# Performance work log

Hardware: AMD Instinct MI355X
Metric: run time of the kernel (lower is better)

The kernel has to match this reference:

```python
import jax, jax.numpy as jnp
import numpy as np

K = 8            # top-k neighbors per channel
BN_EPS = 1e-3    # keras BatchNormalization default


def top_k_features(h, adj, k):
    # h: [N, F], adj: [N, N] (dense). Per node and per channel, take the k
    # largest masked neighbor feature values, then prepend the node's own feature.
    masked = adj[:, None, :] * h.T[None, :, :]        # [N, F, N]
    topk = jax.lax.top_k(masked, k)[0]                # [N, F, K]
    topk = jnp.transpose(topk, (0, 2, 1))             # [N, K, F]
    return jnp.concatenate([h[:, None, :], topk], axis=1)  # [N, K+1, F]


def conv1d(x, w):
    # x: [N, L, Cin], w: [kw, Cin, Cout], VALID 1D conv
    return jax.lax.conv_general_dilated(x, w, (1,), 'VALID',
                                        dimension_numbers=('NWC', 'WIO', 'NWC'))


def batchnorm(x, gamma, beta, mean, var):
    return gamma * (x - mean) * jax.lax.rsqrt(var + BN_EPS) + beta


def setup_inputs():
    key = jax.random.key(0)
    ks = jax.random.split(key, 16)
    N, Fin, H, Cout, NF = 1600, 1433, 32, 7, 8
    x = jax.random.normal(ks[0], (N, Fin), jnp.float32)
    # sparse binary adjacency, avg degree ~16
    adj = (jax.random.uniform(ks[1], (N, N)) < 0.01).astype(jnp.float32)
    mask = jax.random.uniform(ks[2], (N,)) < 0.5

    def g(k, shape, fan_in):
        return jax.random.normal(k, shape, jnp.float32) * (1.0 / np.sqrt(fan_in))

    W0 = g(ks[3], (Fin, H), Fin)                 # DenseConvolution (GCN) weight
    # LGConv block 1: F=32 -> mid (32+8)//2=20 -> 8; kernels 5,5 reduce 9->5->1
    W1a = g(ks[4], (5, 32, 20), 5 * 32)
    W1b = g(ks[5], (5, 20, NF), 5 * 20)
    # LGConv block 2: F=40 -> mid (40+8)//2=24 -> 8
    W2a = g(ks[6], (5, 40, 24), 5 * 40)
    W2b = g(ks[7], (5, 24, NF), 5 * 24)
    Wout = g(ks[8], (H + 2 * NF, Cout), H + 2 * NF)  # 48 -> 7
    bn = {}
    for i, kk in ((1, 9), (2, 12)):
        bn[f'g{i}'] = 1.0 + 0.1 * jax.random.normal(ks[kk], (NF,), jnp.float32)
        bn[f'b{i}'] = 0.1 * jax.random.normal(ks[kk + 1], (NF,), jnp.float32)
        bn[f'm{i}'] = 0.1 * jax.random.normal(ks[kk + 2], (NF,), jnp.float32)
        bn[f'v{i}'] = jax.random.uniform(ks[kk], (NF,), jnp.float32, 0.5, 1.5)
    return {'x': x, 'adj': adj, 'W0': W0, 'W1a': W1a, 'W1b': W1b,
            'W2a': W2a, 'W2b': W2b, 'Wout': Wout,
            'g1': bn['g1'], 'b1': bn['b1'], 'm1': bn['m1'], 'v1': bn['v1'],
            'g2': bn['g2'], 'b2': bn['b2'], 'm2': bn['m2'], 'v2': bn['v2'],
            'mask': mask}


def reference(x, adj, W0, W1a, W1b, W2a, W2b, Wout,
              g1, b1, m1, v1, g2, b2, m2, v2, mask):
    # inference mode: dropout = identity
    h = adj @ (x @ W0)                                # GCN layer, hidden=32
    for Wa, Wb, g, b, m, v in ((W1a, W1b, g1, b1, m1, v1),
                               (W2a, W2b, g2, b2, m2, v2)):
        t = top_k_features(h, adj, K)                 # [N, K+1, F]
        c = conv1d(t, Wa)                             # [N, 5, mid]
        c = conv1d(c, Wb)[:, 0, :]                    # [N, 8]
        c = batchnorm(c, g, b, m, v)
        h = jnp.concatenate([h, c], axis=-1)          # 32 -> 40 -> 48
    logits = adj @ (h @ Wout)                         # [N, 7]
    # Mask layer (boolean_mask); static-shape variant: zero out masked rows
    return jnp.where(mask[:, None], logits, 0.0)
```

## Files before the change

kernel.cpp:

```cpp
#include <hip/hip_runtime.h>


constexpr int NN   = 1600;
constexpr int FIN  = 1433;
constexpr int HGCN = 32;
constexpr int NBS  = 96;
constexpr float BN_EPS = 1e-3f;

constexpr int KS    = 16;
constexpr int CHUNK = 90;
constexpr int BM    = 32;
constexpr int SXS   = 92;
constexpr int RB    = NN / BM;
constexpr int CSRB  = 400;
constexpr int K1B   = CSRB + 1 + RB * KS;
constexpr int GB    = 256;
constexpr int NT    = 512;

__device__ __forceinline__ void astore(float* p, float v) {
    __hip_atomic_store(p, v, __ATOMIC_RELAXED, __HIP_MEMORY_SCOPE_AGENT);
}

__device__ __forceinline__ void gbar(int* cnt, int* rel, int phase) {
    __syncthreads();
    if (blockIdx.x == 0) {
        if (threadIdx.x == 0)
            __hip_atomic_fetch_add(&cnt[phase * 1024], 1,
                                   __ATOMIC_RELAXED, __HIP_MEMORY_SCOPE_AGENT);
        if (threadIdx.x < 32) {
            int* slot = &cnt[phase * 1024 + threadIdx.x * 32];
            while (__hip_atomic_load(slot, __ATOMIC_RELAXED,
                                     __HIP_MEMORY_SCOPE_AGENT) < (GB / 32))
                __builtin_amdgcn_s_sleep(1);
        }
        if (threadIdx.x == 0)
            __hip_atomic_store(&rel[phase], 1,
                               __ATOMIC_RELAXED, __HIP_MEMORY_SCOPE_AGENT);
    } else {
        if (threadIdx.x == 0) {
            __hip_atomic_fetch_add(&cnt[phase * 1024 + (blockIdx.x & 31) * 32], 1,
                                   __ATOMIC_RELAXED, __HIP_MEMORY_SCOPE_AGENT);
            while (__hip_atomic_load(&rel[phase], __ATOMIC_RELAXED,
                                     __HIP_MEMORY_SCOPE_AGENT) == 0)
                __builtin_amdgcn_s_sleep(1);
        }
    }
    __syncthreads();
}

__global__ __launch_bounds__(256) void k1(const float* __restrict__ x,
                                          const float* __restrict__ W0,
                                          const float* __restrict__ adj,
                                          const float* __restrict__ W1a,
                                          const float* __restrict__ W2a,
                                          int* __restrict__ deg,
                                          unsigned short* __restrict__ nbr,
                                          const unsigned char* __restrict__ mb,
                                          int* __restrict__ flag,
                                          float* __restrict__ wsT1,
                                          float* __restrict__ wsT2,
                                          float* __restrict__ h0) {
    __shared__ float sx[BM][SXS];
    __shared__ float sw[CHUNK * HGCN];
    int b = blockIdx.x, t = threadIdx.x;

    if (b < CSRB) {
        int lane = t & 63;
        int row  = b * 4 + (t >> 6);
        const float*  ar  = adj + (size_t)row * NN;
        const float4* ar4 = (const float4*)ar;
        unsigned short* nb = nbr + (size_t)row * NBS;
        int cnt = 0;
        #pragma unroll
        for (int it = 0; it < 6; ++it) {
            float4 v = ar4[it * 64 + lane];
            int base = it * 256 + 4 * lane;
            #pragma unroll
            for (int c = 0; c < 4; ++c) {
                float vc = (c == 0) ? v.x : (c == 1) ? v.y : (c == 2) ? v.z : v.w;
                bool p = (vc != 0.0f);
                unsigned long long m = __ballot(p);
                if (p) {
                    int off = cnt + __popcll(m & ((1ull << lane) - 1ull));
                    if (off < NBS) nb[off] = (unsigned short)(base + c);
                }
                cnt += __popcll(m);
            }
        }
        {
            float v = ar[1536 + lane];
            bool p = (v != 0.0f);
            unsigned long long m = __ballot(p);
            if (p) {
                int off = cnt + __popcll(m & ((1ull << lane) - 1ull));
                if (off < NBS) nb[off] = (unsigned short)(1536 + lane);
            }
            cnt += __popcll(m);
        }
        if (lane == 0) deg[row] = cnt < NBS ? cnt : NBS;
        return;
    }

    if (b == CSRB) {
        if (t < 64) {
            int lane = t;
            bool odd = false, flt = false;
            for (int i = lane; i < NN; i += 64) {
                unsigned char v = mb[i];
                if (v) {
                    int r = i & 3;
                    if (r != 0) odd = true;
                    if (r >= 2 && (v == 0x3F || v == 0x80)) flt = true;
                }
            }
            unsigned long long mo = __ballot(odd);
            unsigned long long mf = __ballot(flt);
            if (lane == 0) *flag = mf ? 2 : (mo ? 1 : 0);
        }
        for (int s = t; s < 5 * 32 * 20; s += 256) {
            int kw = s / 640, r = s - kw * 640, ci = r / 20, o = r - ci * 20;
            wsT1[(kw * 20 + o) * 36 + ci] = W1a[s];
        }
        for (int s = t; s < 5 * 40 * 24; s += 256) {
            int kw = s / 960, r = s - kw * 960, ci = r / 24, o = r - ci * 24;
            wsT2[(kw * 24 + o) * 44 + ci] = W2a[s];
        }
        return;
    }

    int tile = b - (CSRB + 1);
    int rb   = tile % RB;
    int ks   = tile / RB;
    int lane = t & 31;
    int row0 = rb * BM;
    int k0   = ks * CHUNK;
    int vk   = FIN - k0; if (vk > CHUNK) vk = CHUNK;

    {
        int g = t >> 5;
        #pragma unroll
        for (int j = 0; j < 4; ++j) {
            int r = g + 8 * j;
            const float* xr = x + (size_t)(row0 + r) * FIN + k0;
            #pragma unroll
            for (int m = 0; m < 3; ++m) {
                int k = lane + 32 * m;
                if (k < CHUNK) sx[r][k] = (k < vk) ? xr[k] : 0.0f;
            }
        }
    }
    {
        const float4* w4  = (const float4*)(W0 + (size_t)k0 * HGCN);
        float4*       sw4 = (float4*)sw;
        int vf4 = vk * 8;
        for (int i = t; i < CHUNK * 8; i += 256)
            sw4[i] = (i < vf4) ? w4[i] : make_float4(0.f, 0.f, 0.f, 0.f);
    }
    __syncthreads();

    int col = lane;
    int rq  = t >> 5;
    float acc0 = 0.f, acc1 = 0.f, acc2 = 0.f, acc3 = 0.f;
    #pragma unroll 4
    for (int kk = 0; kk < 88; kk += 4) {
        float4 a0 = *(const float4*)&sx[rq     ][kk];
        float4 a1 = *(const float4*)&sx[rq +  8][kk];
        float4 a2 = *(const float4*)&sx[rq + 16][kk];
        float4 a3 = *(const float4*)&sx[rq + 24][kk];
        float w0v = sw[(kk + 0) * HGCN + col];
        float w1v = sw[(kk + 1) * HGCN + col];
        float w2v = sw[(kk + 2) * HGCN + col];
        float w3v = sw[(kk + 3) * HGCN + col];
        acc0 += a0.x * w0v + a0.y * w1v + a0.z * w2v + a0.w * w3v;
        acc1 += a1.x * w0v + a1.y * w1v + a1.z * w2v + a1.w * w3v;
        acc2 += a2.x * w0v + a2.y * w1v + a2.z * w2v + a2.w * w3v;
        acc3 += a3.x * w0v + a3.y * w1v + a3.z * w2v + a3.w * w3v;
    }
    #pragma unroll
    for (int kk = 88; kk < CHUNK; ++kk) {
        float wv = sw[kk * HGCN + col];
        acc0 += sx[rq     ][kk] * wv;
        acc1 += sx[rq +  8][kk] * wv;
        acc2 += sx[rq + 16][kk] * wv;
        acc3 += sx[rq + 24][kk] * wv;
    }

    atomicAdd(&h0[(row0 + rq     ) * HGCN + col], acc0);
    atomicAdd(&h0[(row0 + rq +  8) * HGCN + col], acc1);
    atomicAdd(&h0[(row0 + rq + 16) * HGCN + col], acc2);
    atomicAdd(&h0[(row0 + rq + 24) * HGCN + col], acc3);
}

template<int F, int MID, int FP>
__device__ __forceinline__ void lgconv_phase(int b, int wave, int lane,
        const int* __restrict__ deg, const unsigned short* __restrict__ nbr,
        const float* sWt, const float* __restrict__ Wb,
        const float* __restrict__ g, const float* __restrict__ bb,
        const float* __restrict__ mm, const float* __restrict__ vv,
        const float* __restrict__ h32, const float* __restrict__ c1in,
        float* __restrict__ outbuf, float* T, float* C1) {
    int row = b + 256 * wave;
    if (row >= NN) return;
    int d = deg[row];
    const unsigned short* nb = nbr + (size_t)row * NBS;

    if (lane < F) {
        float t0=0.f,t1=0.f,t2=0.f,t3=0.f,t4=0.f,t5=0.f,t6=0.f,t7=0.f;
        #define BUBBLE(val_) { float val=val_, c;                       \
            c = t0; t0 = fmaxf(c, val); val = fminf(c, val);            \
            c = t1; t1 = fmaxf(c, val); val = fminf(c, val);            \
            c = t2; t2 = fmaxf(c, val); val = fminf(c, val);            \
            c = t3; t3 = fmaxf(c, val); val = fminf(c, val);            \
            c = t4; t4 = fmaxf(c, val); val = fminf(c, val);            \
            c = t5; t5 = fmaxf(c, val); val = fminf(c, val);            \
            c = t6; t6 = fmaxf(c, val); val = fminf(c, val);            \
            c = t7; t7 = fmaxf(c, val); val = fminf(c, val); }
        #define LDV(n_) ((F == 32) ? h32[(n_) * HGCN + lane]            \
            : ((lane < 32) ? h32[(n_) * HGCN + lane] : c1in[(n_) * 8 + (lane - 32)]))
        int it = 0;
        for (; it + 8 <= d; it += 8) {
            float v[8];
            #pragma unroll
            for (int j = 0; j < 8; ++j) v[j] = LDV((int)nb[it + j]);
            #pragma unroll
            for (int j = 0; j < 8; ++j) BUBBLE(v[j]);
        }
        for (; it < d; ++it) BUBBLE(LDV((int)nb[it]));
        T[0*F+lane] = LDV(row);
        T[1*F+lane] = t0; T[2*F+lane] = t1; T[3*F+lane] = t2; T[4*F+lane] = t3;
        T[5*F+lane] = t4; T[6*F+lane] = t5; T[7*F+lane] = t6; T[8*F+lane] = t7;
        #undef LDV
        #undef BUBBLE
    }
    for (int oi = lane; oi < 5 * MID; oi += 64) {
        int p = oi / MID, o = oi - p * MID;
        float ax = 0.f, ay = 0.f, az = 0.f, aw = 0.f;
        #pragma unroll
        for (int kw = 0; kw < 5; ++kw) {
            const float4* t4 = (const float4*)&T[(p + kw) * F];
            const float4* w4 = (const float4*)&sWt[(kw * MID + o) * FP];
            #pragma unroll
            for (int q = 0; q < F / 4; ++q) {
                float4 tv = t4[q], wv = w4[q];
                ax += tv.x * wv.x; ay += tv.y * wv.y;
                az += tv.z * wv.z; aw += tv.w * wv.w;
            }
        }
        C1[p * MID + o] = (ax + ay) + (az + aw);
    }
    if (lane < 8) {
        float acc = 0.f;
        #pragma unroll
        for (int kw = 0; kw < 5; ++kw)
            for (int ci = 0; ci < MID; ++ci)
                acc += C1[kw * MID + ci] * Wb[(kw * MID + ci) * 8 + lane];
        float y = g[lane] * (acc - mm[lane]) * rsqrtf(vv[lane] + BN_EPS) + bb[lane];
        astore(&outbuf[row * 8 + lane], y);
    }
}

__global__ __launch_bounds__(NT) void k2(
        const int* __restrict__ deg, const unsigned short* __restrict__ nbr,
        const float* __restrict__ h0,
        float* __restrict__ h32, float* __restrict__ c1, float* __restrict__ c2,
        const float* __restrict__ wsT1, const float* __restrict__ wsT2,
        const float* __restrict__ W1b,
        const float* __restrict__ g1, const float* __restrict__ b1,
        const float* __restrict__ m1, const float* __restrict__ v1,
        const float* __restrict__ W2b,
        const float* __restrict__ g2, const float* __restrict__ b2,
        const float* __restrict__ m2, const float* __restrict__ v2,
        const float* __restrict__ Wout, const void* __restrict__ mask,
        const int* __restrict__ flag, int* __restrict__ cntrel,
        float* __restrict__ out) {
    __shared__ float sWt1[3600];
    __shared__ float sWt2[5280];
    __shared__ float T   [8][360];
    __shared__ float C1s [8][120];
    __shared__ float sfin[8][48];
    int t = threadIdx.x, b = blockIdx.x;
    int wave = t >> 6, lane = t & 63;
    int* cnt = cntrel;
    int* rel = cntrel + 4 * 1024;

    {
        const float4* s1 = (const float4*)wsT1;
        const float4* s2 = (const float4*)wsT2;
        float4* d1 = (float4*)sWt1;
        float4* d2 = (float4*)sWt2;
        for (int i = t; i < 900;  i += NT) d1[i] = s1[i];
        for (int i = t; i < 1320; i += NT) d2[i] = s2[i];
    }

    {
        int row = b + 256 * (t >> 5);
        if (row < NN) {
            int f = t & 31;
            int d = deg[row];
            const unsigned short* nb = nbr + (size_t)row * NBS;
            float acc = 0.f;
            int it = 0;
            for (; it + 8 <= d; it += 8) {
                float v[8];
                #pragma unroll
                for (int j = 0; j < 8; ++j) v[j] = h0[(int)nb[it + j] * HGCN + f];
                #pragma unroll
                for (int j = 0; j < 8; ++j) acc += v[j];
            }
            for (; it < d; ++it) acc += h0[(int)nb[it] * HGCN + f];
            astore(&h32[row * HGCN + f], acc);
        }
    }
    gbar(cnt, rel, 0);

    lgconv_phase<32, 20, 36>(b, wave, lane, deg, nbr, sWt1, W1b,
                             g1, b1, m1, v1, h32, nullptr, c1,
                             T[wave], C1s[wave]);
    gbar(cnt, rel, 1);

    lgconv_phase<40, 24, 44>(b, wave, lane, deg, nbr, sWt2, W2b,
                             g2, b2, m2, v2, h32, c1, c2,
                             T[wave], C1s[wave]);
    gbar(cnt, rel, 2);

    {
        int row = b + 256 * wave;
        if (row < NN) {
            int d = deg[row];
            const unsigned short* nb = nbr + (size_t)row * NBS;
            if (lane < 48) {
                #define LDF(n_) ((lane < 32) ? h32[(n_) * HGCN + lane]      \
                    : (lane < 40) ? c1[(n_) * 8 + (lane - 32)]              \
                                  : c2[(n_) * 8 + (lane - 40)])
                float acc = 0.f;
                int it = 0;
                for (; it + 8 <= d; it += 8) {
                    float v[8];
                    #pragma unroll
                    for (int j = 0; j < 8; ++j) v[j] = LDF((int)nb[it + j]);
                    #pragma unroll
                    for (int j = 0; j < 8; ++j) acc += v[j];
                }
                for (; it < d; ++it) acc += LDF((int)nb[it]);
                sfin[wave][lane] = acc;
                #undef LDF
            }
            if (lane < 7) {
                float acc = 0.f;
                #pragma unroll
                for (int k = 0; k < 48; ++k)
                    acc += sfin[wave][k] * Wout[k * 7 + lane];
                int fl = *flag;
                bool mk;
                if (fl == 2)      mk = ((const float*)mask)[row] != 0.0f;
                else if (fl == 1) mk = ((const unsigned char*)mask)[row] != 0;
                else              mk = ((const int*)mask)[row] != 0;
                out[row * 7 + lane] = mk ? acc : 0.0f;
            }
        }
    }
}

extern "C" void kernel_launch(void* const* d_in, const int* in_sizes, int n_in,
                              void* d_out, int out_size, void* d_ws, size_t ws_size,
                              hipStream_t stream) {
    const float* x    = (const float*)d_in[0];
    const float* adj  = (const float*)d_in[1];
    const float* W0   = (const float*)d_in[2];
    const float* W1a  = (const float*)d_in[3];
    const float* W1b  = (const float*)d_in[4];
    const float* W2a  = (const float*)d_in[5];
    const float* W2b  = (const float*)d_in[6];
    const float* Wout = (const float*)d_in[7];
    const float* g1 = (const float*)d_in[8];
    const float* b1 = (const float*)d_in[9];
    const float* m1 = (const float*)d_in[10];
    const float* v1 = (const float*)d_in[11];
    const float* g2 = (const float*)d_in[12];
    const float* b2 = (const float*)d_in[13];
    const float* m2 = (const float*)d_in[14];
    const float* v2 = (const float*)d_in[15];
    const void*  mask = d_in[16];

    char* ws = (char*)d_ws;
    int*            cntrel = (int*)(ws + 0);
    float*          h0     = (float*)(ws + 20480);
    int*            flag   = (int*)(ws + 225280);
    int*            deg    = (int*)(ws + 225792);
    unsigned short* nbr    = (unsigned short*)(ws + 232192);
    float*          h32    = (float*)(ws + 539392);
    float*          c1     = (float*)(ws + 744192);
    float*          c2     = (float*)(ws + 795392);
    float*          wsT1   = (float*)(ws + 846592);
    float*          wsT2   = (float*)(ws + 860992);

    float* out = (float*)d_out;

    hipMemsetAsync(ws, 0, 225280, stream);
    k1<<<K1B, 256, 0, stream>>>(x, W0, adj, W1a, W2a, deg, nbr,
                                (const unsigned char*)mask, flag, wsT1, wsT2, h0);
    k2<<<GB, NT, 0, stream>>>(deg, nbr, h0, h32, c1, c2, wsT1, wsT2,
                              W1b, g1, b1, m1, v1,
                              W2b, g2, b2, m2, v2,
                              Wout, mask, flag, cntrel, out);
}
```

Baseline: 56.02 us.

## Reassociate final GCN aggregation via per-node Wout projection; flag-based grid barrier

Result: faster. 52.70 us (-5.9%).

```diff
diff --git a/kernel.cpp b/kernel.cpp
--- a/kernel.cpp
+++ b/kernel.cpp
@@ -20,29 +20,28 @@
 __device__ __forceinline__ void astore(float* p, float v) {
     __hip_atomic_store(p, v, __ATOMIC_RELAXED, __HIP_MEMORY_SCOPE_AGENT);
 }
-
-__device__ __forceinline__ void gbar(int* cnt, int* rel, int phase) {
+__device__ __forceinline__ void astorei(int* p, int v) {
+    __hip_atomic_store(p, v, __ATOMIC_RELAXED, __HIP_MEMORY_SCOPE_AGENT);
+}
+__device__ __forceinline__ int aloadi(const int* p) {
+    return __hip_atomic_load(p, __ATOMIC_RELAXED, __HIP_MEMORY_SCOPE_AGENT);
+}
+
+__device__ __forceinline__ void gbar(int* cntrel, int phase) {
+    int* cnt = cntrel + phase * GB;
+    int* rel = cntrel + 896 + phase;
     __syncthreads();
     if (blockIdx.x == 0) {
-        if (threadIdx.x == 0)
-            __hip_atomic_fetch_add(&cnt[phase * 1024], 1,
-                                   __ATOMIC_RELAXED, __HIP_MEMORY_SCOPE_AGENT);
-        if (threadIdx.x < 32) {
-            int* slot = &cnt[phase * 1024 + threadIdx.x * 32];
-            while (__hip_atomic_load(slot, __ATOMIC_RELAXED,
-                                     __HIP_MEMORY_SCOPE_AGENT) < (GB / 32))
-                __builtin_amdgcn_s_sleep(1);
-        }
-        if (threadIdx.x == 0)
-            __hip_atomic_store(&rel[phase], 1,
-                               __ATOMIC_RELAXED, __HIP_MEMORY_SCOPE_AGENT);
+        int s = threadIdx.x;
+        if (s >= 1 && s < GB) {
+            while (aloadi(&cnt[s]) == 0) __builtin_amdgcn_s_sleep(1);
+        }
+        __syncthreads();
+        if (threadIdx.x == 0) astorei(rel, 1);
     } else {
         if (threadIdx.x == 0) {
-            __hip_atomic_fetch_add(&cnt[phase * 1024 + (blockIdx.x & 31) * 32], 1,
-                                   __ATOMIC_RELAXED, __HIP_MEMORY_SCOPE_AGENT);
-            while (__hip_atomic_load(&rel[phase], __ATOMIC_RELAXED,
-                                     __HIP_MEMORY_SCOPE_AGENT) == 0)
-                __builtin_amdgcn_s_sleep(1);
+            astorei(&cnt[blockIdx.x], 1);
+            while (aloadi(rel) == 0) __builtin_amdgcn_s_sleep(1);
         }
     }
     __syncthreads();
@@ -191,14 +190,15 @@
     atomicAdd(&h0[(row0 + rq + 24) * HGCN + col], acc3);
 }
 
-template<int F, int MID, int FP>
+template<int F, int MID, int FP, bool WRITEZ>
 __device__ __forceinline__ void lgconv_phase(int b, int wave, int lane,
         const int* __restrict__ deg, const unsigned short* __restrict__ nbr,
         const float* sWt, const float* __restrict__ Wb,
         const float* __restrict__ g, const float* __restrict__ bb,
         const float* __restrict__ mm, const float* __restrict__ vv,
         const float* __restrict__ h32, const float* __restrict__ c1in,
-        float* __restrict__ outbuf, float* T, float* C1) {
+        const float* __restrict__ Wout,
+        float* __restrict__ outbuf, float* T, float* C1, float* sz) {
     int row = b + 256 * wave;
     if (row >= NN) return;
     int d = deg[row];
@@ -255,14 +255,27 @@
             for (int ci = 0; ci < MID; ++ci)
                 acc += C1[kw * MID + ci] * Wb[(kw * MID + ci) * 8 + lane];
         float y = g[lane] * (acc - mm[lane]) * rsqrtf(vv[lane] + BN_EPS) + bb[lane];
-        astore(&outbuf[row * 8 + lane], y);
+        if (WRITEZ) sz[lane] = y;
+        else        astore(&outbuf[row * 8 + lane], y);
+    }
+    if (WRITEZ) {
+        if (lane < 8) {
+            float z = 0.f;
+            if (lane < 7) {
+                #pragma unroll
+                for (int k = 0; k < 40; ++k) z += T[k] * Wout[k * 7 + lane];
+                #pragma unroll
+                for (int j = 0; j < 8; ++j)  z += sz[j] * Wout[(40 + j) * 7 + lane];
+            }
+            astore(&outbuf[row * 8 + lane], z);
+        }
     }
 }
 
 __global__ __launch_bounds__(NT) void k2(
         const int* __restrict__ deg, const unsigned short* __restrict__ nbr,
         const float* __restrict__ h0,
-        float* __restrict__ h32, float* __restrict__ c1, float* __restrict__ c2,
+        float* __restrict__ h32, float* __restrict__ c1, float* __restrict__ zbuf,
         const float* __restrict__ wsT1, const float* __restrict__ wsT2,
         const float* __restrict__ W1b,
         const float* __restrict__ g1, const float* __restrict__ b1,
@@ -277,11 +290,9 @@
     __shared__ float sWt2[5280];
     __shared__ float T   [8][360];
     __shared__ float C1s [8][120];
-    __shared__ float sfin[8][48];
+    __shared__ float szs [8][8];
     int t = threadIdx.x, b = blockIdx.x;
     int wave = t >> 6, lane = t & 63;
-    int* cnt = cntrel;
-    int* rel = cntrel + 4 * 1024;
 
     {
         const float4* s1 = (const float4*)wsT1;
@@ -311,45 +322,31 @@
             astore(&h32[row * HGCN + f], acc);
         }
     }
-    gbar(cnt, rel, 0);
-
-    lgconv_phase<32, 20, 36>(b, wave, lane, deg, nbr, sWt1, W1b,
-                             g1, b1, m1, v1, h32, nullptr, c1,
-                             T[wave], C1s[wave]);
-    gbar(cnt, rel, 1);
-
-    lgconv_phase<40, 24, 44>(b, wave, lane, deg, nbr, sWt2, W2b,
-                             g2, b2, m2, v2, h32, c1, c2,
-                             T[wave], C1s[wave]);
-    gbar(cnt, rel, 2);
+    gbar(cntrel, 0);
+
+    lgconv_phase<32, 20, 36, false>(b, wave, lane, deg, nbr, sWt1, W1b,
+                                    g1, b1, m1, v1, h32, nullptr, Wout, c1,
+                                    T[wave], C1s[wave], szs[wave]);
+    gbar(cntrel, 1);
+
+    lgconv_phase<40, 24, 44, true>(b, wave, lane, deg, nbr, sWt2, W2b,
+                                   g2, b2, m2, v2, h32, c1, Wout, zbuf,
+                                   T[wave], C1s[wave], szs[wave]);
+    gbar(cntrel, 2);
 
     {
         int row = b + 256 * wave;
         if (row < NN) {
             int d = deg[row];
             const unsigned short* nb = nbr + (size_t)row * NBS;
-            if (lane < 48) {
-                #define LDF(n_) ((lane < 32) ? h32[(n_) * HGCN + lane]      \
-                    : (lane < 40) ? c1[(n_) * 8 + (lane - 32)]              \
-                                  : c2[(n_) * 8 + (lane - 40)])
-                float acc = 0.f;
-                int it = 0;
-                for (; it + 8 <= d; it += 8) {
-                    float v[8];
-                    #pragma unroll
-                    for (int j = 0; j < 8; ++j) v[j] = LDF((int)nb[it + j]);
-                    #pragma unroll
-                    for (int j = 0; j < 8; ++j) acc += v[j];
-                }
-                for (; it < d; ++it) acc += LDF((int)nb[it]);
-                sfin[wave][lane] = acc;
-                #undef LDF
-            }
+            int ng = lane >> 3, c = lane & 7;
+            float acc = 0.f;
+            for (int it = ng; it < d; it += 8)
+                acc += zbuf[(int)nb[it] * 8 + c];
+            acc += __shfl_xor(acc, 8);
+            acc += __shfl_xor(acc, 16);
+            acc += __shfl_xor(acc, 32);
             if (lane < 7) {
-                float acc = 0.f;
-                #pragma unroll
-                for (int k = 0; k < 48; ++k)
-                    acc += sfin[wave][k] * Wout[k * 7 + lane];
                 int fl = *flag;
                 bool mk;
                 if (fl == 2)      mk = ((const float*)mask)[row] != 0.0f;
@@ -390,7 +387,7 @@
     unsigned short* nbr    = (unsigned short*)(ws + 232192);
     float*          h32    = (float*)(ws + 539392);
     float*          c1     = (float*)(ws + 744192);
-    float*          c2     = (float*)(ws + 795392);
+    float*          zbuf   = (float*)(ws + 795392);
     float*          wsT1   = (float*)(ws + 846592);
     float*          wsT2   = (float*)(ws + 860992);
 
@@ -399,7 +396,7 @@
     hipMemsetAsync(ws, 0, 225280, stream);
     k1<<<K1B, 256, 0, stream>>>(x, W0, adj, W1a, W2a, deg, nbr,
                                 (const unsigned char*)mask, flag, wsT1, wsT2, h0);
-    k2<<<GB, NT, 0, stream>>>(deg, nbr, h0, h32, c1, c2, wsT1, wsT2,
+    k2<<<GB, NT, 0, stream>>>(deg, nbr, h0, h32, c1, zbuf, wsT1, wsT2,
                               W1b, g1, b1, m1, v1,
                               W2b, g2, b2, m2, v2,
                               Wout, mask, flag, cntrel, out);
```
